# Performance work log

Hardware: AMD Instinct MI355X
Metric: run time of the kernel (lower is better)

The kernel has to match this reference:

```python
import jax, jax.numpy as jnp
import numpy as np

N_FFT = 2048
FQ = N_FFT // 2 + 1  # 1025

def _build_bands():
    f, interval = 0, 4
    groups = []
    while f < FQ:
        end = min(f + interval, FQ)
        groups.append(list(range(f, end)))
        f = end
        if interval < 32:
            interval += 1
    K = len(groups)                      # 45 bands
    W = max(len(g) for g in groups)      # 32 max band width
    idx = np.full((K, W), N_FFT // 2, dtype=np.int32)  # dummy pad index 1024
    mask = np.zeros((K, W), dtype=np.float32)
    for k, g in enumerate(groups):
        idx[k, :len(g)] = g
        mask[k, :len(g)] = 1.0
    return idx, mask

_IDX, _MASK = _build_bands()
K, W = _IDX.shape

def setup_inputs() -> dict:
    key = jax.random.key(0)
    k1, k2, k3 = jax.random.split(key, 3)
    B, C, T = 8, 4, 1000
    D = 384
    IN = W * C  # 128
    bound = 1.0 / np.sqrt(IN)
    x = jax.random.normal(k1, (B, C, T, FQ), dtype=jnp.float32)
    w_pre = jax.random.uniform(k2, (K, IN, D), dtype=jnp.float32, minval=-bound, maxval=bound)
    b_pre = jnp.zeros((K, D), dtype=jnp.float32)
    bound2 = 1.0 / np.sqrt(D)
    w_post = jax.random.uniform(k3, (K, D, IN), dtype=jnp.float32, minval=-bound2, maxval=bound2)
    b_post = jnp.zeros((K, IN), dtype=jnp.float32)
    return {"x": x, "w_pre": w_pre, "b_pre": b_pre, "w_post": w_post, "b_post": b_post}

def reference(x, w_pre, b_pre, w_post, b_post):
    idx_flat = jnp.asarray(_IDX.reshape(-1))          # (K*W,) int32
    mask_flat = jnp.asarray(_MASK.reshape(-1))        # (K*W,)
    B, C, T, F = x.shape
    # --- transform: gather + per-band linear ---
    xg = x[..., idx_flat] * mask_flat                 # (B,C,T,K*W)
    xg = xg.reshape(B, C, T, K, W)
    xg = jnp.transpose(xg, (0, 2, 3, 4, 1)).reshape(B, T, K, W * C)  # b t k (w c)
    h = jnp.einsum('btki,kio->btko', xg, w_pre) + b_pre               # (B,T,K,D)
    # --- inverse_transform: per-band linear + scatter-add OLA ---
    y = jnp.einsum('btkd,kdo->btko', h, w_post) + b_post              # (B,T,K,W*C)
    y = y.reshape(B, T, K, W, C)
    y = jnp.transpose(y, (0, 4, 1, 2, 3)).reshape(B, C, T, K * W)     # b c t (k w)
    y = y * mask_flat
    buf = jnp.zeros((B, C, T, F), dtype=x.dtype).at[..., idx_flat].add(y)
    ola_window = jnp.ones((F,), dtype=x.dtype)
    return buf / ola_window
```

## Files before the change

kernel.cpp:

```cpp
#include <hip/hip_runtime.h>
#include <hip/hip_bf16.h>

typedef float f32x4 __attribute__((ext_vector_type(4)));
typedef __bf16 bf16x8 __attribute__((ext_vector_type(8)));
typedef __bf16 bf16x4 __attribute__((ext_vector_type(4)));
typedef unsigned int u32;
typedef const __attribute__((address_space(1))) u32* gas_u32;
typedef __attribute__((address_space(3))) u32* las_u32;

#define NPRE (45L * 384 * 128)

__global__ __launch_bounds__(256) void prep_weights(
    const float* __restrict__ w_pre, const float* __restrict__ w_post,
    __bf16* __restrict__ wpreT, __bf16* __restrict__ wpostT) {
  __shared__ float tile[128 * 65];
  const int tid = threadIdx.x;
  const int bid = blockIdx.x;
  if (bid < 270) {
    int k = bid / 6, o0 = (bid % 6) * 64;
#pragma unroll
    for (int it = 0; it < 32; ++it) {
      int i = it * 4 + (tid >> 6);
      tile[i * 65 + (tid & 63)] = w_pre[((long)(k * 128 + i)) * 384 + o0 + (tid & 63)];
    }
    __syncthreads();
#pragma unroll
    for (int it = 0; it < 8; ++it) {
      int lin = it * 256 + tid;
      int ol = lin >> 5;
      int ip0 = (lin & 31) * 4;
      bf16x4 v;
#pragma unroll
      for (int jj = 0; jj < 4; ++jj) {
        int ip = ip0 + jj;
        int irow = ((ip & 31) << 2) + (ip >> 5);
        v[jj] = (__bf16)tile[irow * 65 + ol];
      }
      *(bf16x4*)(wpreT + ((long)(k * 384 + o0 + ol)) * 128 + ip0) = v;
    }
  } else {
    int r = bid - 270;
    int k = r / 3, s = r % 3;
#pragma unroll
    for (int h = 0; h < 2; ++h) {
      if (h) __syncthreads();
#pragma unroll
      for (int it = 0; it < 32; ++it) {
        int dl = it * 2 + (tid >> 7);
        int i = tid & 127;
        tile[dl * 129 + i] = w_post[((long)(k * 384 + s * 128 + h * 64 + dl)) * 128 + i];
      }
      __syncthreads();
#pragma unroll
      for (int it = 0; it < 8; ++it) {
        int lin = it * 256 + tid;
        int np = lin >> 4;
        int pl0 = h * 64 + (lin & 15) * 4;
        int i_n = ((np & 31) << 2) + (np >> 5);
        int w0 = pl0 & 31, qq = w0 >> 3, j0 = w0 & 7;
        int dbase = (pl0 & ~31) - h * 64 + (qq << 2);
        bf16x4 v;
#pragma unroll
        for (int jj = 0; jj < 4; ++jj) {
          int j = j0 + jj;
          int dloc = dbase + ((j >> 2) << 4) + (j & 3);
          v[jj] = (__bf16)tile[dloc * 129 + i_n];
        }
        *(bf16x4*)(wpostT + (((long)(k * 3 + s)) * 128 + np) * 128 + pl0) = v;
      }
    }
  }
}

__global__ __launch_bounds__(512, 4) void band_mlp(
    const float* __restrict__ x,
    const float* __restrict__ b_pre, const float* __restrict__ b_post,
    const __bf16* __restrict__ wpreT, const __bf16* __restrict__ wpostT,
    float* __restrict__ out) {
  __shared__ __bf16 sA[128 * 128];
  __shared__ __bf16 sW2[2][64 * 128];

  const int tid = threadIdx.x;
  const int bid = blockIdx.x;

  int k, tile;
  if (bid < 2520) {
    int s = bid & 7, seq = bid >> 3;
    int bi = seq / 63;
    tile = seq - bi * 63;
    k = bi * 8 + s;
  } else {
    int r = bid - 2520;
    k = 40 + r / 63;
    tile = r - (k - 40) * 63;
  }

  const int f0 = (k <= 28) ? (k * (k + 7)) / 2 : 490 + 32 * (k - 28);
  int len = (4 + k < 32) ? 4 + k : 32;
  if (len > 1025 - f0) len = 1025 - f0;

  const __bf16* wpre_k  = wpreT  + (long)k * 384 * 128;
  const __bf16* wpost_k = wpostT + (long)k * 384 * 128;

  auto stage_half = [&](int p) {
    const __bf16* src = (p < 6 ? wpre_k : wpost_k) + (long)(p < 6 ? p : p - 6) * 8192;
    __bf16* dst = sW2[p & 1];
#pragma unroll
    for (int u = 0; u < 2; ++u) {
      int lin = u * 512 + tid;
      int row = lin >> 4, gp = lin & 15;
      int gl = gp ^ (row & 7);
      __builtin_amdgcn_global_load_lds((gas_u32)(const void*)(src + row * 128 + gl * 8),
                                       (las_u32)(void*)(dst + lin * 8), 16, 0, 0);
    }
  };

  stage_half(0);

  {
    const int grp = tid >> 5, l32 = tid & 31;
    for (int it = 0; it < 32; ++it) {
      int idx = it * 16 + grp;
      int row = idx >> 2, c = idx & 3;
      int m = tile * 128 + row;
      int b = m / 1000, t = m - b * 1000;
      float v = (l32 < len && m < 8000)
                    ? x[((long)(b * 4 + c) * 1000 + t) * 1025 + f0 + l32] : 0.0f;
      int col = c * 32 + l32;
      int gr = (col >> 3) ^ (row & 7);
      sA[row * 128 + gr * 8 + (col & 7)] = (__bf16)v;
    }
  }

  const int lane = tid & 63;
  const int wid = tid >> 6;
  const int l15 = lane & 15;
  const int q = lane >> 4;
  const int m0 = wid * 16;
  const int swz = l15 & 7;

  bf16x8 hA[12];

  __syncthreads();

#pragma unroll
  for (int p = 0; p < 6; ++p) {
    const int s = p >> 1, hf = p & 1;
    stage_half(p + 1);
    f32x4 bias[4];
#pragma unroll
    for (int ot = 0; ot < 4; ++ot)
      bias[ot] = *(const f32x4*)(b_pre + k * 384 + s * 128 + hf * 64 + ot * 16 + q * 4);
    f32x4 accH[4];
#pragma unroll
    for (int ot = 0; ot < 4; ++ot) accH[ot] = (f32x4){0.f, 0.f, 0.f, 0.f};
#pragma unroll
    for (int ch = 0; ch < 4; ++ch) {
      bf16x8 xb = *(const bf16x8*)(sA + (m0 + l15) * 128 + (((ch * 4 + q) ^ swz) * 8));
#pragma unroll
      for (int ot = 0; ot < 4; ++ot) {
        bf16x8 wa = *(const bf16x8*)(sW2[p & 1] + (ot * 16 + l15) * 128 + (((ch * 4 + q) ^ swz) * 8));
        accH[ot] = __builtin_amdgcn_mfma_f32_16x16x32_bf16(wa, xb, accH[ot], 0, 0, 0);
      }
    }
#pragma unroll
    for (int ot = 0; ot < 4; ++ot) {
      int OT = s * 8 + hf * 4 + ot;
#pragma unroll
      for (int r = 0; r < 4; ++r)
        hA[OT >> 1][(OT & 1) * 4 + r] = (__bf16)(accH[ot][r] + bias[ot][r]);
    }
    __syncthreads();
  }

  f32x4 accY[8];
#pragma unroll
  for (int i = 0; i < 8; ++i) accY[i] = (f32x4){0.f, 0.f, 0.f, 0.f};

#pragma unroll
  for (int p = 6; p < 12; ++p) {
    const int j = (p - 6) >> 1, hf = p & 1;
    if (p < 11) stage_half(p + 1);
#pragma unroll
    for (int cl = 0; cl < 4; ++cl) {
      bf16x8 a2 = hA[j * 4 + cl];
#pragma unroll
      for (int nt = 0; nt < 4; ++nt) {
        bf16x8 wb = *(const bf16x8*)(sW2[p & 1] + (nt * 16 + l15) * 128 + (((cl * 4 + q) ^ swz) * 8));
        accY[hf * 4 + nt] = __builtin_amdgcn_mfma_f32_16x16x32_bf16(a2, wb, accY[hf * 4 + nt], 0, 0, 0);
      }
    }
    if (p < 11) __syncthreads();
  }

  float bp[8];
#pragma unroll
  for (int nt = 0; nt < 8; ++nt) {
    int n = nt * 16 + l15;
    bp[nt] = b_post[k * 128 + ((n & 31) << 2) + (n >> 5)];
  }
  long obase[4];
  int mrow[4];
#pragma unroll
  for (int r = 0; r < 4; ++r) {
    int m = tile * 128 + m0 + q * 4 + r;
    mrow[r] = m;
    int b = m / 1000, t = m - b * 1000;
    obase[r] = (long)(b * 4) * 1025000 + (long)t * 1025 + f0;
  }
#pragma unroll
  for (int nt = 0; nt < 8; ++nt) {
    int n = nt * 16 + l15;
    int w = n & 31, c = n >> 5;
    if (w < len) {
#pragma unroll
      for (int r = 0; r < 4; ++r)
        if (mrow[r] < 8000)
          out[obase[r] + (long)c * 1025000 + w] = accY[nt][r] + bp[nt];
    }
  }
}

extern "C" void kernel_launch(void* const* d_in, const int* in_sizes, int n_in,
                              void* d_out, int out_size, void* d_ws, size_t ws_size,
                              hipStream_t stream) {
  const float* x      = (const float*)d_in[0];
  const float* w_pre  = (const float*)d_in[1];
  const float* b_pre  = (const float*)d_in[2];
  const float* w_post = (const float*)d_in[3];
  const float* b_post = (const float*)d_in[4];
  float* out = (float*)d_out;

  __bf16* wpreT  = (__bf16*)d_ws;
  __bf16* wpostT = (__bf16*)((char*)d_ws + NPRE * 2);

  prep_weights<<<405, 256, 0, stream>>>(w_pre, w_post, wpreT, wpostT);
  band_mlp<<<2835, 512, 0, stream>>>(x, b_pre, b_post, wpreT, wpostT, out);
}
```

Measured before the change: 468.1 us.

## Triple-buffer weight staging, fold pre-bias into post-bias, vectorize input gather

Folds b_pre through w_post into a combined output bias computed in the prep kernel, which removes the per-phase bias loads and adds. Replaces the two double buffers with one triple-buffered LDS region reused for the input tile. Weight loads are issued two stages ahead, using explicit waitcnt and a single barrier per stage. The input gather now uses float4 loads with a bounds-checked scalar fallback, and the x fragments are kept in registers. The trade-off is more in-flight loads and hand-written synchronisation, plus a small serial bias-folding loop in the prep kernel.

```diff
diff --git a/kernel.cpp b/kernel.cpp
--- a/kernel.cpp
+++ b/kernel.cpp
@@ -9,9 +9,13 @@
 typedef __attribute__((address_space(3))) u32* las_u32;
 
 #define NPRE (45L * 384 * 128)
+#define X_TOT (32800L * 1025)
+
+__device__ float g_bias2[45 * 128];
 
 __global__ __launch_bounds__(256) void prep_weights(
     const float* __restrict__ w_pre, const float* __restrict__ w_post,
+    const float* __restrict__ b_pre, const float* __restrict__ b_post,
     __bf16* __restrict__ wpreT, __bf16* __restrict__ wpostT) {
   __shared__ float tile[128 * 65];
   const int tid = threadIdx.x;
@@ -38,7 +42,7 @@
       }
       *(bf16x4*)(wpreT + ((long)(k * 384 + o0 + ol)) * 128 + ip0) = v;
     }
-  } else {
+  } else if (bid < 405) {
     int r = bid - 270;
     int k = r / 3, s = r % 3;
 #pragma unroll
@@ -69,16 +73,24 @@
         *(bf16x4*)(wpostT + (((long)(k * 3 + s)) * 128 + np) * 128 + pl0) = v;
       }
     }
+  } else {
+    int k = bid - 405;
+    int n = tid;
+    if (n < 128) {
+      float acc = b_post[k * 128 + n];
+      for (int d = 0; d < 384; ++d)
+        acc += b_pre[k * 384 + d] * w_post[((long)k * 384 + d) * 128 + n];
+      g_bias2[k * 128 + n] = acc;
+    }
   }
 }
 
 __global__ __launch_bounds__(512, 4) void band_mlp(
     const float* __restrict__ x,
-    const float* __restrict__ b_pre, const float* __restrict__ b_post,
     const __bf16* __restrict__ wpreT, const __bf16* __restrict__ wpostT,
     float* __restrict__ out) {
-  __shared__ __bf16 sA[128 * 128];
-  __shared__ __bf16 sW2[2][64 * 128];
+  __shared__ __bf16 sB[3 * 64 * 128];
+  __bf16* const sA = sB;
 
   const int tid = threadIdx.x;
   const int bid = blockIdx.x;
@@ -103,8 +115,9 @@
   const __bf16* wpost_k = wpostT + (long)k * 384 * 128;
 
   auto stage_half = [&](int p) {
-    const __bf16* src = (p < 6 ? wpre_k : wpost_k) + (long)(p < 6 ? p : p - 6) * 8192;
-    __bf16* dst = sW2[p & 1];
+    const __bf16* src = (p < 6) ? (wpre_k + (long)p * 8192)
+                                : (wpost_k + (long)(p - 6) * 8192);
+    __bf16* dst = sB + (p % 3) * 8192;
 #pragma unroll
     for (int u = 0; u < 2; ++u) {
       int lin = u * 512 + tid;
@@ -115,20 +128,31 @@
     }
   };
 
-  stage_half(0);
-
   {
-    const int grp = tid >> 5, l32 = tid & 31;
-    for (int it = 0; it < 32; ++it) {
-      int idx = it * 16 + grp;
-      int row = idx >> 2, c = idx & 3;
+#pragma unroll
+    for (int it = 0; it < 8; ++it) {
+      int unit = it * 512 + tid;
+      int row = unit >> 5, rem = unit & 31;
+      int c = rem >> 3, l8 = rem & 7;
       int m = tile * 128 + row;
       int b = m / 1000, t = m - b * 1000;
-      float v = (l32 < len && m < 8000)
-                    ? x[((long)(b * 4 + c) * 1000 + t) * 1025 + f0 + l32] : 0.0f;
-      int col = c * 32 + l32;
-      int gr = (col >> 3) ^ (row & 7);
-      sA[row * 128 + gr * 8 + (col & 7)] = (__bf16)v;
+      long gi = ((long)(b * 4 + c) * 1000 + t) * 1025 + f0 + l8 * 4;
+      f32x4 v = (f32x4){0.f, 0.f, 0.f, 0.f};
+      if (m < 8000) {
+        if (l8 * 4 + 4 <= len && gi + 4 <= X_TOT) {
+          v = *(const f32x4*)(x + gi);
+        } else {
+#pragma unroll
+          for (int j = 0; j < 4; ++j)
+            if (l8 * 4 + j < len && gi + j < X_TOT) v[j] = x[gi + j];
+        }
+      }
+      int col0 = c * 32 + l8 * 4;
+      int gr = (col0 >> 3) ^ (row & 7);
+      bf16x4 bv;
+#pragma unroll
+      for (int j = 0; j < 4; ++j) bv[j] = (__bf16)v[j];
+      *(bf16x4*)(sA + row * 128 + gr * 8 + (col0 & 7)) = bv;
     }
   }
 
@@ -139,65 +163,68 @@
   const int m0 = wid * 16;
   const int swz = l15 & 7;
 
+  __syncthreads();
+
+  bf16x8 xb[4];
+#pragma unroll
+  for (int ch = 0; ch < 4; ++ch)
+    xb[ch] = *(const bf16x8*)(sA + (m0 + l15) * 128 + (((ch * 4 + q) ^ swz) * 8));
+
+  __syncthreads();
+
+  stage_half(0);
+  stage_half(1);
+
   bf16x8 hA[12];
-
-  __syncthreads();
-
-#pragma unroll
-  for (int p = 0; p < 6; ++p) {
-    const int s = p >> 1, hf = p & 1;
-    stage_half(p + 1);
-    f32x4 bias[4];
-#pragma unroll
-    for (int ot = 0; ot < 4; ++ot)
-      bias[ot] = *(const f32x4*)(b_pre + k * 384 + s * 128 + hf * 64 + ot * 16 + q * 4);
-    f32x4 accH[4];
-#pragma unroll
-    for (int ot = 0; ot < 4; ++ot) accH[ot] = (f32x4){0.f, 0.f, 0.f, 0.f};
-#pragma unroll
-    for (int ch = 0; ch < 4; ++ch) {
-      bf16x8 xb = *(const bf16x8*)(sA + (m0 + l15) * 128 + (((ch * 4 + q) ^ swz) * 8));
+  f32x4 accY[8];
+
+#pragma unroll
+  for (int p = 0; p < 12; ++p) {
+    if (p == 11) asm volatile("s_waitcnt vmcnt(0) lgkmcnt(0)" ::: "memory");
+    else         asm volatile("s_waitcnt vmcnt(2) lgkmcnt(0)" ::: "memory");
+    __builtin_amdgcn_s_barrier();
+    __builtin_amdgcn_sched_barrier(0);
+    if (p < 10) stage_half(p + 2);
+    const __bf16* buf = sB + (p % 3) * 8192;
+    if (p < 6) {
+#pragma unroll
+      for (int ot = 0; ot < 4; ++ot) accY[ot] = (f32x4){0.f, 0.f, 0.f, 0.f};
+#pragma unroll
+      for (int ch = 0; ch < 4; ++ch) {
+#pragma unroll
+        for (int ot = 0; ot < 4; ++ot) {
+          bf16x8 wa = *(const bf16x8*)(buf + (ot * 16 + l15) * 128 + (((ch * 4 + q) ^ swz) * 8));
+          accY[ot] = __builtin_amdgcn_mfma_f32_16x16x32_bf16(wa, xb[ch], accY[ot], 0, 0, 0);
+        }
+      }
 #pragma unroll
       for (int ot = 0; ot < 4; ++ot) {
-        bf16x8 wa = *(const bf16x8*)(sW2[p & 1] + (ot * 16 + l15) * 128 + (((ch * 4 + q) ^ swz) * 8));
-        accH[ot] = __builtin_amdgcn_mfma_f32_16x16x32_bf16(wa, xb, accH[ot], 0, 0, 0);
-      }
-    }
-#pragma unroll
-    for (int ot = 0; ot < 4; ++ot) {
-      int OT = s * 8 + hf * 4 + ot;
-#pragma unroll
-      for (int r = 0; r < 4; ++r)
-        hA[OT >> 1][(OT & 1) * 4 + r] = (__bf16)(accH[ot][r] + bias[ot][r]);
-    }
-    __syncthreads();
-  }
-
-  f32x4 accY[8];
-#pragma unroll
-  for (int i = 0; i < 8; ++i) accY[i] = (f32x4){0.f, 0.f, 0.f, 0.f};
-
-#pragma unroll
-  for (int p = 6; p < 12; ++p) {
-    const int j = (p - 6) >> 1, hf = p & 1;
-    if (p < 11) stage_half(p + 1);
-#pragma unroll
-    for (int cl = 0; cl < 4; ++cl) {
-      bf16x8 a2 = hA[j * 4 + cl];
-#pragma unroll
-      for (int nt = 0; nt < 4; ++nt) {
-        bf16x8 wb = *(const bf16x8*)(sW2[p & 1] + (nt * 16 + l15) * 128 + (((cl * 4 + q) ^ swz) * 8));
-        accY[hf * 4 + nt] = __builtin_amdgcn_mfma_f32_16x16x32_bf16(a2, wb, accY[hf * 4 + nt], 0, 0, 0);
-      }
-    }
-    if (p < 11) __syncthreads();
+        int OT = p * 4 + ot;
+#pragma unroll
+        for (int r = 0; r < 4; ++r)
+          hA[OT >> 1][(OT & 1) * 4 + r] = (__bf16)accY[ot][r];
+      }
+    } else {
+      const int pm = p - 6, s2 = pm >> 1, hf = pm & 1;
+#pragma unroll
+      for (int cl = 0; cl < 4; ++cl) {
+        bf16x8 a2 = hA[s2 * 4 + cl];
+#pragma unroll
+        for (int nt = 0; nt < 4; ++nt) {
+          bf16x8 wb = *(const bf16x8*)(buf + (nt * 16 + l15) * 128 + (((cl * 4 + q) ^ swz) * 8));
+          f32x4 cin = (s2 == 0 && cl == 0) ? (f32x4){0.f, 0.f, 0.f, 0.f}
+                                           : accY[hf * 4 + nt];
+          accY[hf * 4 + nt] = __builtin_amdgcn_mfma_f32_16x16x32_bf16(a2, wb, cin, 0, 0, 0);
+        }
+      }
+    }
   }
 
   float bp[8];
 #pragma unroll
   for (int nt = 0; nt < 8; ++nt) {
     int n = nt * 16 + l15;
-    bp[nt] = b_post[k * 128 + ((n & 31) << 2) + (n >> 5)];
+    bp[nt] = g_bias2[k * 128 + ((n & 31) << 2) + (n >> 5)];
   }
   long obase[4];
   int mrow[4];
@@ -234,6 +261,6 @@
   __bf16* wpreT  = (__bf16*)d_ws;
   __bf16* wpostT = (__bf16*)((char*)d_ws + NPRE * 2);
 
-  prep_weights<<<405, 256, 0, stream>>>(w_pre, w_post, wpreT, wpostT);
-  band_mlp<<<2835, 512, 0, stream>>>(x, b_pre, b_post, wpreT, wpostT, out);
+  prep_weights<<<450, 256, 0, stream>>>(w_pre, w_post, b_pre, b_post, wpreT, wpostT);
+  band_mlp<<<2835, 512, 0, stream>>>(x, wpreT, wpostT, out);
 }
```

Measured after the change: 386.9 us. 1.21x faster.
